# Kernel optimization log

Measured on AMD Instinct MI355X. Metric: run time of the kernel, lower is better.

Reference implementation:

```python
import jax, jax.numpy as jnp
import numpy as np

N, E = 50000, 1000000
IN_DIM, HID, OUT = 2, 32, 16
H1, H2 = 4, 1
NEG_SLOPE = 0.2
LN_EPS = 1e-5


def _glorot(key, shape):
    fan_in, fan_out = shape[0], shape[1]
    lim = (6.0 / (fan_in + fan_out)) ** 0.5
    return jax.random.uniform(key, shape, jnp.float32, -lim, lim)


def layer_norm(x, g, b):
    mu = jnp.mean(x, axis=-1, keepdims=True)
    var = jnp.var(x, axis=-1, keepdims=True)
    return (x - mu) * jax.lax.rsqrt(var + LN_EPS) * g + b


def gatv2_conv(x, src, dst, edge_attr, Wl, bl, Wr, br, We, att, bias, H, C):
    # x: (N, F) -> out: (N, C)  (concat=False: mean over heads)
    n = x.shape[0]
    xl = (x @ Wl + bl).reshape(n, H, C)   # source transform
    xr = (x @ Wr + br).reshape(n, H, C)   # destination transform
    e = (edge_attr @ We).reshape(-1, H, C)  # edge feature transform (no bias)
    # per-edge message, LeakyReLU, attention logit
    m = jax.nn.leaky_relu(xl[src] + xr[dst] + e, NEG_SLOPE)  # (E, H, C)
    logit = jnp.einsum('ehc,hc->eh', m, att)                 # (E, H)
    # scatter softmax grouped by destination node
    amax = jax.ops.segment_max(logit, dst, num_segments=n)    # (N, H)
    ex = jnp.exp(logit - amax[dst])                           # (E, H)
    denom = jax.ops.segment_sum(ex, dst, num_segments=n)      # (N, H)
    alpha = ex / (denom[dst] + 1e-16)                         # (E, H)
    # weighted scatter-aggregate of source features
    out = jax.ops.segment_sum(alpha[:, :, None] * xl[src], dst, num_segments=n)  # (N, H, C)
    return jnp.mean(out, axis=1) + bias


def setup_inputs() -> dict:
    key = jax.random.key(0)
    ks = jax.random.split(key, 16)
    x = jax.random.normal(ks[0], (N, IN_DIM), jnp.float32)
    edge_index = jax.random.randint(ks[1], (2, E), 0, N, jnp.int64)
    edge_attr = jax.random.normal(ks[2], (E, 1), jnp.float32)
    inp = {
        'x': x, 'edge_index': edge_index, 'edge_attr': edge_attr,
        # layer 1 (in=2 -> H1*HID)
        'W1l': _glorot(ks[3], (IN_DIM, H1 * HID)), 'b1l': jnp.zeros((H1 * HID,), jnp.float32),
        'W1r': _glorot(ks[4], (IN_DIM, H1 * HID)), 'b1r': jnp.zeros((H1 * HID,), jnp.float32),
        'We1': _glorot(ks[5], (1, H1 * HID)),
        'att1': _glorot(ks[6], (H1, HID)),
        'bias1': jnp.zeros((HID,), jnp.float32),
        'g1': jnp.ones((HID,), jnp.float32), 'beta1': jnp.zeros((HID,), jnp.float32),
        # layer 2 (HID -> H2*OUT)
        'W2l': _glorot(ks[7], (HID, H2 * OUT)), 'b2l': jnp.zeros((H2 * OUT,), jnp.float32),
        'W2r': _glorot(ks[8], (HID, H2 * OUT)), 'b2r': jnp.zeros((H2 * OUT,), jnp.float32),
        'We2': _glorot(ks[9], (1, H2 * OUT)),
        'att2': _glorot(ks[10], (H2, OUT)),
        'bias2': jnp.zeros((OUT,), jnp.float32),
        'g2': jnp.ones((OUT,), jnp.float32), 'beta2': jnp.zeros((OUT,), jnp.float32),
    }
    return inp


def reference(x, edge_index, edge_attr, W1l, b1l, W1r, b1r, We1, att1, bias1, g1, beta1,
              W2l, b2l, W2r, b2r, We2, att2, bias2, g2, beta2):
    src, dst = edge_index[0], edge_index[1]
    h = gatv2_conv(x, src, dst, edge_attr, W1l, b1l, W1r, b1r, We1, att1, bias1, H1, HID)
    h = jax.nn.elu(layer_norm(h, g1, beta1))  # dropout p=0.0 -> identity
    z = gatv2_conv(h, src, dst, edge_attr, W2l, b2l, W2r, b2r, We2, att2, bias2, H2, OUT)
    return layer_norm(z, g2, beta2)
```

## Files before the change

kernel.cpp:

```cpp
#include <hip/hip_runtime.h>
#include <hip/hip_bf16.h>
#include <math.h>

typedef __hip_bfloat16 bf16;

__device__ __forceinline__ float b2f(bf16 v) { return __bfloat162float(v); }
__device__ __forceinline__ bf16  f2b(float v) { return __float2bfloat16(v); }

template<int F32>
__device__ __forceinline__ float ldf(const void* p, int i) {
    return F32 ? ((const float*)p)[i] : b2f(((const bf16*)p)[i]);
}
template<int F32>
__device__ __forceinline__ void ldx(const void* x, int s, float& x0, float& x1) {
    if (F32) { float2 v = ((const float2*)x)[s]; x0 = v.x; x1 = v.y; }
    else {
        unsigned u = ((const unsigned*)x)[s];
        x0 = __uint_as_float((u & 0xFFFFu) << 16);
        x1 = __uint_as_float(u & 0xFFFF0000u);
    }
}
__device__ __forceinline__ unsigned f2b_hi(float f) {
    unsigned u = __float_as_uint(f);
    u += 0x7FFFu + ((u >> 16) & 1u);
    return u & 0xFFFF0000u;
}
template<int P4>
__device__ __forceinline__ void ldrec(const void* csr, int k, int& s, float& a) {
    if (P4) {
        unsigned u = ((const unsigned*)csr)[k];
        s = (int)(u & 0xFFFFu);
        a = __uint_as_float(u & 0xFFFF0000u);
    } else {
        uint2 r = ((const uint2*)csr)[k];
        s = (int)r.x;
        a = __uint_as_float(r.y);
    }
}
__device__ __forceinline__ float sclamp(float v, float lim) {
    return fminf(fmaxf(v, -lim), lim);
}
template<int CTRL>
__device__ __forceinline__ float dpp_add(float v) {
    int t = __builtin_amdgcn_update_dpp(0, __float_as_int(v), CTRL, 0xF, 0xF, true);
    return v + __int_as_float(t);
}
__device__ __forceinline__ float red16(float v) {
    v = dpp_add<0xB1>(v);
    v = dpp_add<0x4E>(v);
    v = dpp_add<0x124>(v);
    v = dpp_add<0x128>(v);
    return v;
}

#define NEG_SLOPE 0.2f
#define LN_EPS 1e-5f
#define SCAN_TILE 1024
#define ACHUNK 2048
#define EBMAX 512
#define SCAP 8192

__device__ __forceinline__ int ld_idx(const int* ei, long long pos, int is64, int N) {
    int v = is64 ? ei[2 * pos] : ei[pos];
    return min(max(v, 0), N - 1);
}
__device__ __forceinline__ int calc_is64(const int* ei) {
    int hi = 0, nz = 0;
    #pragma unroll
    for (int i = 0; i < 8; ++i) { hi |= ei[2 * i + 1]; nz |= ei[2 * i]; }
    return (hi == 0 && nz != 0) ? 1 : 0;
}
__device__ __forceinline__ int calc_isf32(const unsigned short* xu) {
    int pl = 0;
    for (int i = 0; i < 32; ++i) {
        unsigned ex = (xu[2 * i] >> 7) & 0xFF;
        if (ex >= 100 && ex <= 140) pl++;
    }
    return (pl >= 24) ? 0 : 1;
}


template<int F32>
__device__ void bina1_body(const int* __restrict__ ei, const void* __restrict__ attr,
                           int E, int N, int is64,
                           unsigned* __restrict__ binned4, unsigned char* __restrict__ binnedb,
                           int* __restrict__ cntm, int* __restrict__ locm,
                           int* cnt, int* incl, int* cur,
                           unsigned* stage4, unsigned char* stageb) {
    int tid = threadIdx.x, b = blockIdx.x;
    cnt[tid] = 0;
    __syncthreads();
    int i0 = b * ACHUNK;
    int iend = min(i0 + ACHUNK, E);
    unsigned rec[8]; int bk[8], lo[8];
    #pragma unroll
    for (int r = 0; r < 8; ++r) {
        int i = i0 + tid + r * 256;
        bk[r] = -1;
        if (i < iend) {
            int d = ld_idx(ei, (long long)E + i, is64, N);
            int s = ld_idx(ei, (long long)i, is64, N);
            float a = ldf<F32>(attr, i);
            rec[r] = f2b_hi(a) | (unsigned)s;
            bk[r] = d >> 8;
            lo[r] = d & 255;
            atomicAdd(&cnt[bk[r]], 1);
        }
    }
    __syncthreads();
    incl[tid] = cnt[tid];
    __syncthreads();
    for (int off = 1; off < 256; off <<= 1) {
        int u = (tid >= off) ? incl[tid - off] : 0;
        __syncthreads();
        incl[tid] += u;
        __syncthreads();
    }
    cur[tid] = incl[tid] - cnt[tid];
    __syncthreads();
    #pragma unroll
    for (int r = 0; r < 8; ++r) {
        if (bk[r] >= 0) {
            int p = atomicAdd(&cur[bk[r]], 1);
            stage4[p] = rec[r];
            stageb[p] = (unsigned char)lo[r];
        }
    }
    __syncthreads();
    int n = iend - i0;
    for (int i = tid; i < n; i += 256) {
        binned4[(size_t)b * ACHUNK + i] = stage4[i];
        binnedb[(size_t)b * ACHUNK + i] = stageb[i];
    }
    cntm[b * 256 + tid] = cnt[tid];
    locm[b * 256 + tid] = incl[tid] - cnt[tid];
}

__global__ __launch_bounds__(256) void bina1_kernel(const int* __restrict__ ei,
                                                    const void* __restrict__ attr,
                                                    const unsigned short* __restrict__ xu,
                                                    int E, int N, int* __restrict__ flags,
                                                    unsigned* __restrict__ binned4,
                                                    unsigned char* __restrict__ binnedb,
                                                    int* __restrict__ cntm,
                                                    int* __restrict__ locm) {
    __shared__ int cnt[256], incl[256], cur[256];
    __shared__ unsigned stage4[ACHUNK];
    __shared__ unsigned char stageb[ACHUNK];
    __shared__ int sflags[2];
    if (threadIdx.x == 0) {
        sflags[0] = calc_is64(ei);
        sflags[1] = calc_isf32(xu);
        if (blockIdx.x == 0) { flags[0] = sflags[0]; flags[1] = sflags[1]; }
    }
    __syncthreads();
    if (sflags[1]) bina1_body<1>(ei, attr, E, N, sflags[0], binned4, binnedb, cntm, locm,
                                 cnt, incl, cur, stage4, stageb);
    else           bina1_body<0>(ei, attr, E, N, sflags[0], binned4, binnedb, cntm, locm,
                                 cnt, incl, cur, stage4, stageb);
}

__global__ __launch_bounds__(256) void sumb_kernel(const int* __restrict__ cntm,
                                                   int* __restrict__ btot, int EB,
                                                   int* __restrict__ rowptr, int N, int E) {
    __shared__ int w[4];
    int B = blockIdx.x, tid = threadIdx.x;
    if (B == 0 && tid == 0) rowptr[N] = E;
    int s = 0;
    for (int j = tid; j < EB; j += 256) s += cntm[j * 256 + B];
    #pragma unroll
    for (int off = 1; off < 64; off <<= 1) s += __shfl_xor(s, off);
    if ((tid & 63) == 0) w[tid >> 6] = s;
    __syncthreads();
    if (tid == 0) btot[B] = w[0] + w[1] + w[2] + w[3];
}

__global__ __launch_bounds__(256) void passb_kernel(const unsigned* __restrict__ binned4,
                                                    const unsigned char* __restrict__ binnedb,
                                                    const int* __restrict__ cntm,
                                                    const int* __restrict__ locm,
                                                    const int* __restrict__ btot,
                                                    int* __restrict__ rowptr,
                                                    unsigned* __restrict__ csr,
                                                    int N, int EB, int NB) {
    __shared__ int nc[256], incl[256], cur[256], bsc[256], ebase[256];
    __shared__ int cntl[EBMAX], locl[EBMAX];
    __shared__ unsigned stage4[SCAP];
    __shared__ unsigned char stageb[SCAP];
    __shared__ int stageCnt;
    int B = blockIdx.x, tid = threadIdx.x;
    int v = (tid < NB) ? btot[tid] : 0;
    bsc[tid] = v;
    nc[tid] = 0;
    if (tid == 0) stageCnt = 0;
    for (int j = tid; j < EB; j += 256) {
        cntl[j] = cntm[j * 256 + B];
        locl[j] = locm[j * 256 + B];
    }
    __syncthreads();
    for (int off = 1; off < 256; off <<= 1) {
        int u = (tid >= off) ? bsc[tid - off] : 0;
        __syncthreads();
        bsc[tid] += u;
        __syncthreads();
    }
    ebase[tid] = bsc[tid] - v;
    __syncthreads();
    int base = ebase[B];
    int cntb = btot[B];
    bool fit = (cntb <= SCAP);

    if (fit) {
        for (int j = tid; j < EB; j += 256) {
            int c = cntl[j];
            if (c > 0) {
                int p = atomicAdd(&stageCnt, c);
                const unsigned* s4 = binned4 + (size_t)j * ACHUNK + locl[j];
                const unsigned char* sb = binnedb + (size_t)j * ACHUNK + locl[j];
                for (int i = 0; i < c; ++i) {
                    unsigned r4 = s4[i];
                    unsigned char l = sb[i];
                    stage4[p + i] = r4;
                    stageb[p + i] = l;
                    atomicAdd(&nc[l], 1);
                }
            }
        }
    } else {
        for (int j = tid; j < EB; j += 256) {
            int c = cntl[j];
            const unsigned char* sb = binnedb + (size_t)j * ACHUNK + locl[j];
            for (int i = 0; i < c; ++i) atomicAdd(&nc[sb[i]], 1);
        }
    }
    __syncthreads();
    incl[tid] = nc[tid];
    __syncthreads();
    for (int off = 1; off < 256; off <<= 1) {
        int u = (tid >= off) ? incl[tid - off] : 0;
        __syncthreads();
        incl[tid] += u;
        __syncthreads();
    }
    int excl = incl[tid] - nc[tid];
    int node = (B << 8) + tid;
    if (node < N) rowptr[node] = base + excl;
    cur[tid] = excl;
    __syncthreads();
    if (fit) {
        for (int i = tid; i < cntb; i += 256) {
            int l = stageb[i];
            int p = atomicAdd(&cur[l], 1);
            csr[base + p] = stage4[i];
        }
    } else {
        for (int j = tid; j < EB; j += 256) {
            int c = cntl[j];
            const unsigned* s4 = binned4 + (size_t)j * ACHUNK + locl[j];
            const unsigned char* sb = binnedb + (size_t)j * ACHUNK + locl[j];
            for (int i = 0; i < c; ++i) {
                int p = atomicAdd(&cur[sb[i]], 1);
                csr[base + p] = s4[i];
            }
        }
    }
}


__global__ void hist_kernel(const int* __restrict__ ei, const unsigned short* __restrict__ xu,
                            int E, int N, int* __restrict__ flags, int* __restrict__ cnt) {
    int is64 = calc_is64(ei);
    if (blockIdx.x == 0 && threadIdx.x == 0) {
        flags[0] = is64;
        flags[1] = calc_isf32(xu);
    }
    int e = blockIdx.x * blockDim.x + threadIdx.x;
    if (e >= E) return;
    atomicAdd(&cnt[ld_idx(ei, (long long)E + e, is64, N)], 1);
}

__global__ __launch_bounds__(256) void scan_partial(const int* __restrict__ cnt,
                                                    int* __restrict__ bsum, int N) {
    __shared__ int wsum[4];
    int b = blockIdx.x, tid = threadIdx.x;
    int base = b * SCAN_TILE + tid * 4;
    int4 v = make_int4(0, 0, 0, 0);
    if (base + 3 < N) v = *(const int4*)(cnt + base);
    else {
        if (base + 0 < N) v.x = cnt[base + 0];
        if (base + 1 < N) v.y = cnt[base + 1];
        if (base + 2 < N) v.z = cnt[base + 2];
    }
    int s = v.x + v.y + v.z + v.w;
    #pragma unroll
    for (int off = 1; off < 64; off <<= 1) s += __shfl_xor(s, off);
    if ((tid & 63) == 0) wsum[tid >> 6] = s;
    __syncthreads();
    if (tid == 0) bsum[b] = wsum[0] + wsum[1] + wsum[2] + wsum[3];
}

__global__ __launch_bounds__(256) void scan_final(int* __restrict__ cnt, int* __restrict__ rowptr,
                                                  const int* __restrict__ bsum, int N, int B) {
    __shared__ int tsum[256];
    __shared__ int bpre[256];
    int b = blockIdx.x, tid = threadIdx.x;
    bpre[tid] = (tid < B) ? bsum[tid] : 0;
    int base = b * SCAN_TILE + tid * 4;
    int4 v = make_int4(0, 0, 0, 0);
    if (base + 3 < N) v = *(const int4*)(cnt + base);
    else {
        if (base + 0 < N) v.x = cnt[base + 0];
        if (base + 1 < N) v.y = cnt[base + 1];
        if (base + 2 < N) v.z = cnt[base + 2];
    }
    tsum[tid] = v.x + v.y + v.z + v.w;
    __syncthreads();
    for (int off = 1; off < 256; off <<= 1) {
        int t = (tid >= off) ? tsum[tid - off] : 0;
        int u = (tid >= off) ? bpre[tid - off] : 0;
        __syncthreads();
        tsum[tid] += t;
        bpre[tid] += u;
        __syncthreads();
    }
    int blockpre = (b == 0) ? 0 : bpre[b - 1];
    int o0 = blockpre + ((tid == 0) ? 0 : tsum[tid - 1]);
    int o1 = o0 + v.x, o2 = o1 + v.y, o3 = o2 + v.z;
    if (base + 3 < N) {
        int4 o = make_int4(o0, o1, o2, o3);
        *(int4*)(rowptr + base) = o;
        *(int4*)(cnt + base) = o;
    } else {
        if (base + 0 < N) { rowptr[base + 0] = o0; cnt[base + 0] = o0; }
        if (base + 1 < N) { rowptr[base + 1] = o1; cnt[base + 1] = o1; }
        if (base + 2 < N) { rowptr[base + 2] = o2; cnt[base + 2] = o2; }
    }
    if (b == 0 && tid == 255) rowptr[N] = bpre[255];
}

template<int F32>
__device__ void scatter_body(const int* __restrict__ ei, const void* __restrict__ attr,
                             int E, int N, int is64, int* __restrict__ cursor,
                             uint2* __restrict__ csr) {
    int e = blockIdx.x * blockDim.x + threadIdx.x;
    if (e >= E) return;
    int d = ld_idx(ei, (long long)E + e, is64, N);
    int s = ld_idx(ei, (long long)e, is64, N);
    float av = ldf<F32>(attr, e);
    int pos = atomicAdd(&cursor[d], 1);
    csr[pos] = make_uint2((unsigned)s, __float_as_uint(av));
}

__global__ void scatter_kernel(const int* __restrict__ ei, const void* __restrict__ attr,
                               int E, int N, const int* __restrict__ flags,
                               int* __restrict__ cursor, uint2* __restrict__ csr) {
    if (flags[1]) scatter_body<1>(ei, attr, E, N, flags[0], cursor, csr);
    else          scatter_body<0>(ei, attr, E, N, flags[0], cursor, csr);
}


template<int F32, int P4>
__device__ void agg1_body(
    const int* __restrict__ rowptr, const void* __restrict__ csr,
    const void* __restrict__ x,
    const void* W1l, const void* b1l, const void* W1r, const void* b1r,
    const void* We1, const void* att1, const void* bias1, const void* g1v, const void* beta1,
    bf16* __restrict__ hout, int N) {
    int w0 = __builtin_amdgcn_readfirstlane((blockIdx.x * blockDim.x + threadIdx.x) >> 6);
    int NW = (gridDim.x * blockDim.x) >> 6;
    int lane = threadIdx.x & 63;
    int h = lane >> 4, q = lane & 15;
    int ja = h * 32 + q, jb = ja + 16;

    float wlaA = ldf<F32>(W1l, ja),      wlaB = ldf<F32>(W1l, jb);
    float wlbA = ldf<F32>(W1l, 128 + ja), wlbB = ldf<F32>(W1l, 128 + jb);
    float wraA = ldf<F32>(W1r, ja),      wraB = ldf<F32>(W1r, jb);
    float wrbA = ldf<F32>(W1r, 128 + ja), wrbB = ldf<F32>(W1r, 128 + jb);
    float blA = ldf<F32>(b1l, ja), blB = ldf<F32>(b1l, jb);
    float brA = ldf<F32>(b1r, ja), brB = ldf<F32>(b1r, jb);
    float weA = ldf<F32>(We1, ja), weB = ldf<F32>(We1, jb);
    float atA = ldf<F32>(att1, ja), atB = ldf<F32>(att1, jb);
    float aa4A = 0.4f * atA, aa4B = 0.4f * atB;
    float blbrA = blA + brA, blbrB = blB + brB;
    float P0 = 0.6f * red16(atA * wlaA + atB * wlaB);
    float P1 = 0.6f * red16(atA * wlbA + atB * wlbB);
    float Pw = 0.6f * red16(atA * weA + atB * weB);
    float Q0 = 0.6f * red16(atA * wraA + atB * wraB);
    float Q1 = 0.6f * red16(atA * wrbA + atB * wrbB);
    float Qc = 0.6f * red16(atA * blbrA + atB * blbrB);
    float biasA = ldf<F32>(bias1, q), biasB = ldf<F32>(bias1, q + 16);
    float gA = ldf<F32>(g1v, q), gB = ldf<F32>(g1v, q + 16);
    float beA = ldf<F32>(beta1, q), beB = ldf<F32>(beta1, q + 16);

    for (int n = w0; n < N; n += NW) {
        int beg = rowptr[n], end = rowptr[n + 1];
        float xd0, xd1;
        ldx<F32>(x, n, xd0, xd1);
        float cA = fmaf(xd0, wraA, fmaf(xd1, wrbA, blbrA));
        float cB = fmaf(xd0, wraB, fmaf(xd1, wrbB, blbrB));
        float Kn = fmaf(xd0, Q0, fmaf(xd1, Q1, Qc));
        float S = 0.f, Sx0 = 0.f, Sx1 = 0.f;

        auto edge = [&](float xs0, float xs1, float a) {
            float zA = fmaf(xs0, wlaA, fmaf(xs1, wlbA, fmaf(a, weA, cA)));
            float zB = fmaf(xs0, wlaB, fmaf(xs1, wlbB, fmaf(a, weB, cB)));
            float pabs = red16(fmaf(fabsf(zA), aa4A, fabsf(zB) * aa4B));
            float p = sclamp(fmaf(xs0, P0, fmaf(xs1, P1, fmaf(a, Pw, Kn))) + pabs, 60.f);
            float e = __expf(p);
            S += e;
            Sx0 = fmaf(e, xs0, Sx0);
            Sx1 = fmaf(e, xs1, Sx1);
        };

        int k = beg;
        for (; k + 4 <= end; k += 4) {
            int s0, s1, s2, s3;
            float a0, a1, a2, a3;
            ldrec<P4>(csr, k, s0, a0);
            ldrec<P4>(csr, k + 1, s1, a1);
            ldrec<P4>(csr, k + 2, s2, a2);
            ldrec<P4>(csr, k + 3, s3, a3);
            float p0, p1, q0, q1, r0, r1, t0, t1;
            ldx<F32>(x, s0, p0, p1);
            ldx<F32>(x, s1, q0, q1);
            ldx<F32>(x, s2, r0, r1);
            ldx<F32>(x, s3, t0, t1);
            edge(p0, p1, a0);
            edge(q0, q1, a1);
            edge(r0, r1, a2);
            edge(t0, t1, a3);
        }
        for (; k < end; ++k) {
            int s0; float a0;
            ldrec<P4>(csr, k, s0, a0);
            float p0, p1;
            ldx<F32>(x, s0, p0, p1);
            edge(p0, p1, a0);
        }

        float inv = 1.0f / (S + 1e-16f);
        float R = S * inv, U0 = Sx0 * inv, U1 = Sx1 * inv;
        float outA = fmaf(U0, wlaA, fmaf(U1, wlbA, R * blA));
        float outB = fmaf(U0, wlaB, fmaf(U1, wlbB, R * blB));
        outA += __shfl_xor(outA, 16); outA += __shfl_xor(outA, 32);
        outB += __shfl_xor(outB, 16); outB += __shfl_xor(outB, 32);
        float valA = fmaf(0.25f, outA, biasA);
        float valB = fmaf(0.25f, outB, biasB);
        float mu = red16(valA + valB) * (1.f / 32.f);
        float dA = valA - mu, dB = valB - mu;
        float var = red16(dA * dA + dB * dB) * (1.f / 32.f);
        float rs = rsqrtf(var + LN_EPS);
        float yA = fmaf(dA * rs, gA, beA);
        float yB = fmaf(dB * rs, gB, beB);
        float hA = yA > 0.f ? yA : expm1f(yA);
        float hB = yB > 0.f ? yB : expm1f(yB);
        if (lane < 16) {
            hout[n * 32 + q]      = f2b(hA);
            hout[n * 32 + 16 + q] = f2b(hB);
        }
    }
}

template<int P4>
__global__ __launch_bounds__(256) void agg1_kernel(
    const int* __restrict__ flags,
    const int* __restrict__ rowptr, const void* __restrict__ csr,
    const void* __restrict__ x,
    const void* W1l, const void* b1l, const void* W1r, const void* b1r,
    const void* We1, const void* att1, const void* bias1, const void* g1v, const void* beta1,
    bf16* __restrict__ hout, int N) {
    if (flags[1]) agg1_body<1, P4>(rowptr, csr, x, W1l, b1l, W1r, b1r,
                                   We1, att1, bias1, g1v, beta1, hout, N);
    else          agg1_body<0, P4>(rowptr, csr, x, W1l, b1l, W1r, b1r,
                                   We1, att1, bias1, g1v, beta1, hout, N);
}


template<int F32>
__device__ void node2_body(bf16* __restrict__ hbuf, float* wl, float* wr,
                           const void* W2l, const void* b2l, const void* W2r, const void* b2r,
                           int N) {
    __shared__ float bl[16], br[16];
    int tid = threadIdx.x;
    for (int i = tid; i < 512; i += 256) { wl[i] = ldf<F32>(W2l, i); wr[i] = ldf<F32>(W2r, i); }
    if (tid < 16) { bl[tid] = ldf<F32>(b2l, tid); br[tid] = ldf<F32>(b2r, tid); }
    __syncthreads();
    int n = blockIdx.x * blockDim.x + tid;
    if (n >= N) return;
    float hv[32];
    #pragma unroll
    for (int c = 0; c < 32; ++c) hv[c] = b2f(hbuf[n * 32 + c]);
    float accl[16], accr[16];
    #pragma unroll
    for (int o = 0; o < 16; ++o) { accl[o] = bl[o]; accr[o] = br[o]; }
    #pragma unroll
    for (int c = 0; c < 32; ++c) {
        #pragma unroll
        for (int o = 0; o < 16; ++o) {
            accl[o] = fmaf(hv[c], wl[c * 16 + o], accl[o]);
            accr[o] = fmaf(hv[c], wr[c * 16 + o], accr[o]);
        }
    }
    #pragma unroll
    for (int o = 0; o < 16; ++o) {
        hbuf[n * 32 + o]      = f2b(accl[o]);
        hbuf[n * 32 + 16 + o] = f2b(accr[o]);
    }
}

__global__ __launch_bounds__(256) void node2_kernel(
    const int* __restrict__ flags, bf16* __restrict__ hbuf,
    const void* W2l, const void* b2l, const void* W2r, const void* b2r, int N) {
    __shared__ float wl[512], wr[512];
    if (flags[1]) node2_body<1>(hbuf, wl, wr, W2l, b2l, W2r, b2r, N);
    else          node2_body<0>(hbuf, wl, wr, W2l, b2l, W2r, b2r, N);
}


template<int F32, int P4>
__device__ void agg2_body(
    const int* __restrict__ rowptr, const void* __restrict__ csr,
    const bf16* __restrict__ h2,
    const void* We2, const void* att2, const void* bias2, const void* g2v, const void* beta2,
    void* __restrict__ out, int N) {
    int w0 = __builtin_amdgcn_readfirstlane((blockIdx.x * blockDim.x + threadIdx.x) >> 6);
    int NW = (gridDim.x * blockDim.x) >> 6;
    int lane = threadIdx.x & 63;
    int g = lane >> 4, t = lane & 15;

    float we = ldf<F32>(We2, t), at = ldf<F32>(att2, t);
    float bia = ldf<F32>(bias2, t), gg = ldf<F32>(g2v, t), bb = ldf<F32>(beta2, t);

    for (int n = w0; n < N; n += NW) {
        int beg = rowptr[n], end = rowptr[n + 1];
        float xr = b2f(h2[n * 32 + 16 + t]);

        float S = 0.f, A = 0.f;
        auto edge = [&](float v, float a) {
            float m = fmaf(a, we, v + xr);
            m = fmaxf(m, NEG_SLOPE * m);
            float p = sclamp(red16(m * at), 60.f);
            float e = __expf(p);
            S += e;
            A = fmaf(e, v, A);
        };
        int k = beg + g;
        for (; k + 4 < end; k += 8) {
            int s0, s1; float a0, a1;
            ldrec<P4>(csr, k, s0, a0);
            ldrec<P4>(csr, k + 4, s1, a1);
            float v0 = b2f(h2[s0 * 32 + t]);
            float v1 = b2f(h2[s1 * 32 + t]);
            edge(v0, a0);
            edge(v1, a1);
        }
        if (k < end) {
            int s0; float a0;
            ldrec<P4>(csr, k, s0, a0);
            edge(b2f(h2[s0 * 32 + t]), a0);
        }
        S += __shfl_xor(S, 16); S += __shfl_xor(S, 32);
        A += __shfl_xor(A, 16); A += __shfl_xor(A, 32);
        float val = A / (S + 1e-16f) + bia;

        float mu = red16(val) * (1.f / 16.f);
        float d = val - mu;
        float var = red16(d * d) * (1.f / 16.f);
        float y = fmaf(d * rsqrtf(var + LN_EPS), gg, bb);
        if (lane < 16) {
            if (F32) ((float*)out)[n * 16 + t] = y;
            else     ((bf16*)out)[n * 16 + t] = f2b(y);
        }
    }
}

template<int P4>
__global__ __launch_bounds__(256) void agg2_kernel(
    const int* __restrict__ flags,
    const int* __restrict__ rowptr, const void* __restrict__ csr,
    const bf16* __restrict__ h2,
    const void* We2, const void* att2, const void* bias2, const void* g2v, const void* beta2,
    void* __restrict__ out, int N) {
    if (flags[1]) agg2_body<1, P4>(rowptr, csr, h2, We2, att2, bias2, g2v, beta2, out, N);
    else          agg2_body<0, P4>(rowptr, csr, h2, We2, att2, bias2, g2v, beta2, out, N);
}


static inline size_t align256(size_t x) { return (x + 255) & ~size_t(255); }

extern "C" void kernel_launch(void* const* d_in, const int* in_sizes, int n_in,
                              void* d_out, int out_size, void* d_ws, size_t ws_size,
                              hipStream_t stream) {
    const void* x     = d_in[0];
    const int*  ei    = (const int*)d_in[1];
    const void* eattr = d_in[2];
    const void* W1l   = d_in[3];
    const void* b1l   = d_in[4];
    const void* W1r   = d_in[5];
    const void* b1r   = d_in[6];
    const void* We1   = d_in[7];
    const void* att1  = d_in[8];
    const void* bias1 = d_in[9];
    const void* g1    = d_in[10];
    const void* beta1 = d_in[11];
    const void* W2l   = d_in[12];
    const void* b2l   = d_in[13];
    const void* W2r   = d_in[14];
    const void* b2r   = d_in[15];
    const void* We2   = d_in[16];
    const void* att2  = d_in[17];
    const void* bias2 = d_in[18];
    const void* g2    = d_in[19];
    const void* beta2 = d_in[20];

    const int N = in_sizes[0] / 2;
    const int E = in_sizes[2];
    const int EB = (E + ACHUNK - 1) / ACHUNK;
    const int NB = (N + 255) >> 8;
    const bool p4 = (N <= 65536) && (EB <= EBMAX);

    char* ws = (char*)d_ws;
    size_t off = 0;
    int* flags  = (int*)(ws + off); off += align256(sizeof(int) * 2);
    int* cntm   = (int*)(ws + off); off += align256(sizeof(int) * (size_t)EB * 256);
    int* locm   = (int*)(ws + off); off += align256(sizeof(int) * (size_t)EB * 256);
    int* btot   = (int*)(ws + off); off += align256(sizeof(int) * 256);
    int* rowptr = (int*)(ws + off); off += align256(sizeof(int) * (size_t)(N + 1));
    void* csr   = (void*)(ws + off); off += align256((p4 ? 4u : 8u) * (size_t)E);
    char* big   = (ws + off);
    unsigned* binned4 = (unsigned*)big;
    unsigned char* binnedb = (unsigned char*)(big + align256(sizeof(unsigned) * (size_t)EB * ACHUNK));
    bf16* hbuf = (bf16*)big;

    if (p4) {
        bina1_kernel<<<EB, 256, 0, stream>>>(ei, eattr, (const unsigned short*)x,
                                             E, N, flags, binned4, binnedb, cntm, locm);
        sumb_kernel<<<NB, 256, 0, stream>>>(cntm, btot, EB, rowptr, N, E);
        passb_kernel<<<NB, 256, 0, stream>>>(binned4, binnedb, cntm, locm, btot,
                                             rowptr, (unsigned*)csr, N, EB, NB);
    } else {
        int* cnt = (int*)big;
        hbuf = (bf16*)(big + align256(sizeof(int) * (size_t)N));
        const int B = (N + SCAN_TILE - 1) / SCAN_TILE;
        hipMemsetAsync(cnt, 0, sizeof(int) * (size_t)N, stream);
        hist_kernel<<<(E + 255) / 256, 256, 0, stream>>>(ei, (const unsigned short*)x, E, N, flags, cnt);
        scan_partial<<<B, 256, 0, stream>>>(cnt, cntm, N);
        scan_final<<<B, 256, 0, stream>>>(cnt, rowptr, cntm, N, B);
        scatter_kernel<<<(E + 255) / 256, 256, 0, stream>>>(ei, eattr, E, N, flags, cnt, (uint2*)csr);
    }

    if (p4) agg1_kernel<1><<<2048, 256, 0, stream>>>(flags, rowptr, csr, x,
                                                     W1l, b1l, W1r, b1r, We1, att1,
                                                     bias1, g1, beta1, hbuf, N);
    else    agg1_kernel<0><<<2048, 256, 0, stream>>>(flags, rowptr, csr, x,
                                                     W1l, b1l, W1r, b1r, We1, att1,
                                                     bias1, g1, beta1, hbuf, N);

    node2_kernel<<<(N + 255) / 256, 256, 0, stream>>>(flags, hbuf, W2l, b2l, W2r, b2r, N);

    if (p4) agg2_kernel<1><<<2048, 256, 0, stream>>>(flags, rowptr, csr, hbuf,
                                                     We2, att2, bias2, g2, beta2, d_out, N);
    else    agg2_kernel<0><<<2048, 256, 0, stream>>>(flags, rowptr, csr, hbuf,
                                                     We2, att2, bias2, g2, beta2, d_out, N);
}
```

Before: 209.3 us.

## Fold bucket totals into binning via atomics; widen agg2 to 8 edges per wave

Removes the separate sumb kernel by having each binning block atomically add its per-bucket counts into btot, which is cleared beforehand with a memset. The rowptr[N] write moves into passb. The layer-2 aggregation now has each lane handle two channels through packed bf16x2 loads, so a wave processes 8 edges at a time instead of 4, and the attention reduction needs one fewer DPP step. The costs are a memset launch, global atomic contention on 256 counters, and more shuffle reductions at the end of each node.

```diff
diff --git a/kernel.cpp b/kernel.cpp
--- a/kernel.cpp
+++ b/kernel.cpp
@@ -52,6 +52,12 @@
     v = dpp_add<0x128>(v);
     return v;
 }
+__device__ __forceinline__ float red8(float v) {
+    v = dpp_add<0xB1>(v);
+    v = dpp_add<0x4E>(v);
+    v = dpp_add<0x141>(v);
+    return v;
+}
 
 #define NEG_SLOPE 0.2f
 #define LN_EPS 1e-5f
@@ -85,6 +91,7 @@
                            int E, int N, int is64,
                            unsigned* __restrict__ binned4, unsigned char* __restrict__ binnedb,
                            int* __restrict__ cntm, int* __restrict__ locm,
+                           int* __restrict__ btot,
                            int* cnt, int* incl, int* cur,
                            unsigned* stage4, unsigned char* stageb) {
     int tid = threadIdx.x, b = blockIdx.x;
@@ -132,8 +139,10 @@
         binned4[(size_t)b * ACHUNK + i] = stage4[i];
         binnedb[(size_t)b * ACHUNK + i] = stageb[i];
     }
-    cntm[b * 256 + tid] = cnt[tid];
-    locm[b * 256 + tid] = incl[tid] - cnt[tid];
+    int c = cnt[tid];
+    cntm[b * 256 + tid] = c;
+    locm[b * 256 + tid] = incl[tid] - c;
+    if (c) atomicAdd(&btot[tid], c);
 }
 
 __global__ __launch_bounds__(256) void bina1_kernel(const int* __restrict__ ei,
@@ -143,7 +152,8 @@
                                                     unsigned* __restrict__ binned4,
                                                     unsigned char* __restrict__ binnedb,
                                                     int* __restrict__ cntm,
-                                                    int* __restrict__ locm) {
+                                                    int* __restrict__ locm,
+                                                    int* __restrict__ btot) {
     __shared__ int cnt[256], incl[256], cur[256];
     __shared__ unsigned stage4[ACHUNK];
     __shared__ unsigned char stageb[ACHUNK];
@@ -155,24 +165,9 @@
     }
     __syncthreads();
     if (sflags[1]) bina1_body<1>(ei, attr, E, N, sflags[0], binned4, binnedb, cntm, locm,
-                                 cnt, incl, cur, stage4, stageb);
+                                 btot, cnt, incl, cur, stage4, stageb);
     else           bina1_body<0>(ei, attr, E, N, sflags[0], binned4, binnedb, cntm, locm,
-                                 cnt, incl, cur, stage4, stageb);
-}
-
-__global__ __launch_bounds__(256) void sumb_kernel(const int* __restrict__ cntm,
-                                                   int* __restrict__ btot, int EB,
-                                                   int* __restrict__ rowptr, int N, int E) {
-    __shared__ int w[4];
-    int B = blockIdx.x, tid = threadIdx.x;
-    if (B == 0 && tid == 0) rowptr[N] = E;
-    int s = 0;
-    for (int j = tid; j < EB; j += 256) s += cntm[j * 256 + B];
-    #pragma unroll
-    for (int off = 1; off < 64; off <<= 1) s += __shfl_xor(s, off);
-    if ((tid & 63) == 0) w[tid >> 6] = s;
-    __syncthreads();
-    if (tid == 0) btot[B] = w[0] + w[1] + w[2] + w[3];
+                                 btot, cnt, incl, cur, stage4, stageb);
 }
 
 __global__ __launch_bounds__(256) void passb_kernel(const unsigned* __restrict__ binned4,
@@ -182,13 +177,14 @@
                                                     const int* __restrict__ btot,
                                                     int* __restrict__ rowptr,
                                                     unsigned* __restrict__ csr,
-                                                    int N, int EB, int NB) {
+                                                    int N, int E, int EB, int NB) {
     __shared__ int nc[256], incl[256], cur[256], bsc[256], ebase[256];
     __shared__ int cntl[EBMAX], locl[EBMAX];
     __shared__ unsigned stage4[SCAP];
     __shared__ unsigned char stageb[SCAP];
     __shared__ int stageCnt;
     int B = blockIdx.x, tid = threadIdx.x;
+    if (B == 0 && tid == 0) rowptr[N] = E;
     int v = (tid < NB) ? btot[tid] : 0;
     bsc[tid] = v;
     nc[tid] = 0;
@@ -526,50 +522,57 @@
     int w0 = __builtin_amdgcn_readfirstlane((blockIdx.x * blockDim.x + threadIdx.x) >> 6);
     int NW = (gridDim.x * blockDim.x) >> 6;
     int lane = threadIdx.x & 63;
-    int g = lane >> 4, t = lane & 15;
-
-    float we = ldf<F32>(We2, t), at = ldf<F32>(att2, t);
-    float bia = ldf<F32>(bias2, t), gg = ldf<F32>(g2v, t), bb = ldf<F32>(beta2, t);
+    int g = lane >> 3;
+    int t2 = lane & 7;
+    int c0 = 2 * t2, c1 = c0 + 1;
+
+    float we0 = ldf<F32>(We2, c0), we1 = ldf<F32>(We2, c1);
+    float at0 = ldf<F32>(att2, c0), at1 = ldf<F32>(att2, c1);
+    float bia0 = ldf<F32>(bias2, c0), bia1 = ldf<F32>(bias2, c1);
+    float gg0 = ldf<F32>(g2v, c0), gg1 = ldf<F32>(g2v, c1);
+    float bb0 = ldf<F32>(beta2, c0), bb1 = ldf<F32>(beta2, c1);
 
     for (int n = w0; n < N; n += NW) {
         int beg = rowptr[n], end = rowptr[n + 1];
-        float xr = b2f(h2[n * 32 + 16 + t]);
-
-        float S = 0.f, A = 0.f;
-        auto edge = [&](float v, float a) {
-            float m = fmaf(a, we, v + xr);
-            m = fmaxf(m, NEG_SLOPE * m);
-            float p = sclamp(red16(m * at), 60.f);
+        unsigned uxr = ((const unsigned*)(h2 + (size_t)n * 32 + 16))[t2];
+        float xr0 = __uint_as_float((uxr & 0xFFFFu) << 16);
+        float xr1 = __uint_as_float(uxr & 0xFFFF0000u);
+
+        float S = 0.f, A0 = 0.f, A1 = 0.f;
+        for (int k = beg + g; k < end; k += 8) {
+            int s; float a;
+            ldrec<P4>(csr, k, s, a);
+            unsigned uv = ((const unsigned*)(h2 + (size_t)s * 32))[t2];
+            float v0 = __uint_as_float((uv & 0xFFFFu) << 16);
+            float v1 = __uint_as_float(uv & 0xFFFF0000u);
+            float m0 = fmaf(a, we0, v0 + xr0); m0 = fmaxf(m0, NEG_SLOPE * m0);
+            float m1 = fmaf(a, we1, v1 + xr1); m1 = fmaxf(m1, NEG_SLOPE * m1);
+            float p = sclamp(red8(fmaf(m0, at0, m1 * at1)), 60.f);
             float e = __expf(p);
             S += e;
-            A = fmaf(e, v, A);
-        };
-        int k = beg + g;
-        for (; k + 4 < end; k += 8) {
-            int s0, s1; float a0, a1;
-            ldrec<P4>(csr, k, s0, a0);
-            ldrec<P4>(csr, k + 4, s1, a1);
-            float v0 = b2f(h2[s0 * 32 + t]);
-            float v1 = b2f(h2[s1 * 32 + t]);
-            edge(v0, a0);
-            edge(v1, a1);
-        }
-        if (k < end) {
-            int s0; float a0;
-            ldrec<P4>(csr, k, s0, a0);
-            edge(b2f(h2[s0 * 32 + t]), a0);
-        }
-        S += __shfl_xor(S, 16); S += __shfl_xor(S, 32);
-        A += __shfl_xor(A, 16); A += __shfl_xor(A, 32);
-        float val = A / (S + 1e-16f) + bia;
-
-        float mu = red16(val) * (1.f / 16.f);
-        float d = val - mu;
-        float var = red16(d * d) * (1.f / 16.f);
-        float y = fmaf(d * rsqrtf(var + LN_EPS), gg, bb);
-        if (lane < 16) {
-            if (F32) ((float*)out)[n * 16 + t] = y;
-            else     ((bf16*)out)[n * 16 + t] = f2b(y);
+            A0 = fmaf(e, v0, A0);
+            A1 = fmaf(e, v1, A1);
+        }
+        S  += __shfl_xor(S, 8);  S  += __shfl_xor(S, 16);  S  += __shfl_xor(S, 32);
+        A0 += __shfl_xor(A0, 8); A0 += __shfl_xor(A0, 16); A0 += __shfl_xor(A0, 32);
+        A1 += __shfl_xor(A1, 8); A1 += __shfl_xor(A1, 16); A1 += __shfl_xor(A1, 32);
+        float inv = 1.0f / (S + 1e-16f);
+        float val0 = fmaf(A0, inv, bia0);
+        float val1 = fmaf(A1, inv, bia1);
+
+        float mu = red8(val0 + val1) * (1.f / 16.f);
+        float d0 = val0 - mu, d1 = val1 - mu;
+        float var = red8(d0 * d0 + d1 * d1) * (1.f / 16.f);
+        float rs = rsqrtf(var + LN_EPS);
+        float y0 = fmaf(d0 * rs, gg0, bb0);
+        float y1 = fmaf(d1 * rs, gg1, bb1);
+        if (lane < 8) {
+            if (F32) {
+                ((float2*)out)[(size_t)n * 8 + t2] = make_float2(y0, y1);
+            } else {
+                unsigned pk = (f2b_hi(y0) >> 16) | f2b_hi(y1);
+                ((unsigned*)out)[(size_t)n * 8 + t2] = pk;
+            }
         }
     }
 }
@@ -633,11 +636,11 @@
     bf16* hbuf = (bf16*)big;
 
     if (p4) {
+        hipMemsetAsync(btot, 0, sizeof(int) * 256, stream);
         bina1_kernel<<<EB, 256, 0, stream>>>(ei, eattr, (const unsigned short*)x,
-                                             E, N, flags, binned4, binnedb, cntm, locm);
-        sumb_kernel<<<NB, 256, 0, stream>>>(cntm, btot, EB, rowptr, N, E);
+                                             E, N, flags, binned4, binnedb, cntm, locm, btot);
         passb_kernel<<<NB, 256, 0, stream>>>(binned4, binnedb, cntm, locm, btot,
-                                             rowptr, (unsigned*)csr, N, EB, NB);
+                                             rowptr, (unsigned*)csr, N, E, EB, NB);
     } else {
         int* cnt = (int*)big;
         hbuf = (bf16*)(big + align256(sizeof(int) * (size_t)N));
```

After: 217.4 us. 1.04x slower.
